# Kernel tuning notes

Measured on AMD Instinct MI355X. Metric: run time of the kernel, lower is better.

The kernel has to match this reference:

```python
import jax, jax.numpy as jnp
import numpy as np

INPUT_SIZE, HIDDEN_SIZE, MEMORY_SIZE, SEQ_LEN, THETA = 512, 1024, 256, 4096, 4096.0
BATCH = 8


def _expm(M):
    # scaling-and-squaring Taylor expm (float64), replaces scipy cont2discrete's expm
    nrm = np.linalg.norm(M, 1)
    s = max(0, int(np.ceil(np.log2(max(nrm, 1.0)))) + 4)
    A = M / (2.0 ** s)
    E = np.eye(M.shape[0])
    T = np.eye(M.shape[0])
    for k in range(1, 24):
        T = T @ A / k
        E = E + T
    for _ in range(s):
        E = E @ E
    return E


def _lmu_H():
    # continuous-time Legendre state-space matrices
    Q = np.arange(MEMORY_SIZE, dtype=np.float64).reshape(-1, 1)
    R = (2.0 * Q + 1.0) / THETA
    i, j = np.meshgrid(Q.ravel(), Q.ravel(), indexing="ij")
    A = R * np.where(i < j, -1.0, (-1.0) ** (i - j + 1))
    B = R * (-1.0) ** Q
    # zero-order-hold discretization with dt=1: expm([[A,B],[0,0]])
    aug = np.zeros((MEMORY_SIZE + 1, MEMORY_SIZE + 1))
    aug[:MEMORY_SIZE, :MEMORY_SIZE] = A
    aug[:MEMORY_SIZE, MEMORY_SIZE:] = B
    Md = _expm(aug)
    Ad = Md[:MEMORY_SIZE, :MEMORY_SIZE].astype(np.float32)
    Bd = Md[:MEMORY_SIZE, MEMORY_SIZE:].astype(np.float32)
    # impulse response: H[:, t] = Ad^t @ Bd  (matches torch impulse() in float32)
    H = np.empty((MEMORY_SIZE, SEQ_LEN), dtype=np.float32)
    h = Bd[:, 0]
    for t in range(SEQ_LEN):
        H[:, t] = h
        h = Ad @ h
    return H


def setup_inputs():
    key = jax.random.key(0)
    k1, k2, k3, k4, k5 = jax.random.split(key, 5)
    x = jax.random.normal(k1, (BATCH, SEQ_LEN, INPUT_SIZE), jnp.float32)
    W_u_w = jax.random.normal(k2, (1, INPUT_SIZE), jnp.float32) / np.float32(np.sqrt(INPUT_SIZE))
    W_u_b = jax.random.normal(k3, (1,), jnp.float32) * 0.01
    W_h_w = jax.random.normal(k4, (HIDDEN_SIZE, MEMORY_SIZE + INPUT_SIZE), jnp.float32) / np.float32(np.sqrt(MEMORY_SIZE + INPUT_SIZE))
    W_h_b = jax.random.normal(k5, (HIDDEN_SIZE,), jnp.float32) * 0.01
    H = jnp.asarray(_lmu_H())
    return {"x": x, "W_u_w": W_u_w, "W_u_b": W_u_b, "W_h_w": W_h_w, "W_h_b": W_h_b, "H": H}


def reference(x, W_u_w, W_u_b, W_h_w, W_h_b, H):
    B, S, D = x.shape
    # u_t = relu(W_u x_t)  -> [B, S, 1]
    u = jax.nn.relu(jnp.einsum("bsd,od->bso", x, W_u_w) + W_u_b)
    # FFT long convolution of u with impulse response H (linear conv via 2S padding)
    fft_u = jnp.fft.rfft(u.transpose(0, 2, 1), n=2 * S, axis=-1)  # [B, 1, S+1]
    fft_H = jnp.fft.rfft(H, n=2 * S, axis=-1)                     # [M, S+1]
    m = jnp.fft.irfft(fft_u * fft_H[None], n=2 * S, axis=-1)[:, :, :S]  # [B, M, S]
    m = m.transpose(0, 2, 1)                                      # [B, S, M]
    # h_t = relu(W_h [m_t; x_t])
    h = jax.nn.relu(jnp.einsum("bsk,hk->bsh", jnp.concatenate([m, x], axis=-1), W_h_w) + W_h_b)
    return h, h[:, -1, :]
```

## Files before the change

### kernel.cpp

```cpp
#include <hip/hip_runtime.h>

typedef _Float16 half8 __attribute__((ext_vector_type(8)));
typedef float f32x4 __attribute__((ext_vector_type(4)));

#define SEQ   4096
#define DIN   512
#define HID   1024
#define KMEM  256
#define NB    8
#define KC    768
#define VP    4352
#define OUT_H_ELEMS 33554432ull

__device__ __forceinline__ void load_lds16(const void* g, void* l) {
  __builtin_amdgcn_global_load_lds(
      (const __attribute__((address_space(1))) unsigned int*)g,
      (__attribute__((address_space(3))) unsigned int*)l, 16, 0, 0);
}

__global__ __launch_bounds__(256) void u_kernel(
    const float* __restrict__ x, const float* __restrict__ Wu,
    const float* __restrict__ Wub,
    const float* __restrict__ Hf, const float* __restrict__ Wf,
    _Float16* __restrict__ xh, _Float16* __restrict__ v2,
    _Float16* __restrict__ Hh, _Float16* __restrict__ Wh)
{
  int tid_g = blockIdx.x * 256 + threadIdx.x;
  if (tid_g < KMEM * SEQ) Hh[tid_g] = (_Float16)Hf[tid_g];
  if (tid_g < HID * KC)   Wh[tid_g] = (_Float16)Wf[tid_g];
  if (tid_g < NB * 8 * 256) {
    int b2 = tid_g >> 11, rem = tid_g & 2047, p = rem >> 8, z = rem & 255;
    int t = (z < p) ? z : 4096 + z;
    v2[((size_t)b2 * 8 + p) * VP + t] = (_Float16)0.f;
  }

  int w = threadIdx.x >> 6, lane = threadIdx.x & 63;
  int row = blockIdx.x * 4 + w;
  const float4* xr = (const float4*)(x + (size_t)row * DIN);
  const float4* wr = (const float4*)Wu;
  float4 a0 = xr[lane * 2], a1 = xr[lane * 2 + 1];
  float4 w0 = wr[lane * 2], w1 = wr[lane * 2 + 1];
  float dot = a0.x * w0.x + a0.y * w0.y + a0.z * w0.z + a0.w * w0.w
            + a1.x * w1.x + a1.y * w1.y + a1.z * w1.z + a1.w * w1.w;
  half8 hv;
  hv[0] = (_Float16)a0.x; hv[1] = (_Float16)a0.y;
  hv[2] = (_Float16)a0.z; hv[3] = (_Float16)a0.w;
  hv[4] = (_Float16)a1.x; hv[5] = (_Float16)a1.y;
  hv[6] = (_Float16)a1.z; hv[7] = (_Float16)a1.w;
  *((half8*)(xh + (size_t)row * DIN + lane * 8)) = hv;
  #pragma unroll
  for (int off = 32; off > 0; off >>= 1) dot += __shfl_xor(dot, off);
  float u = dot + Wub[0];
  u = u > 0.f ? u : 0.f;
  if (lane < 8) {
    int s = row & (SEQ - 1), b = row >> 12;
    v2[(size_t)b * 8 * VP + (size_t)lane * VP + (4095 - s + lane)] = (_Float16)u;
  }
}

__global__ __launch_bounds__(256, 3) void conv_kernel(
    const _Float16* __restrict__ Hh, const _Float16* __restrict__ v2,
    _Float16* __restrict__ mh)
{
  __shared__ _Float16 Bs[2][128 * 64];
  __shared__ _Float16 Aw[2][8 * 208];
  int g = blockIdx.x;
  int cb = g & 15;
  int b = cb >> 1, kt = cb & 1;
  int jj = g >> 4;
  int its = (jj < 16) ? jj : (47 - jj);
  int s0 = its * 128, k0 = kt * 128;
  int tid = threadIdx.x;
  int w = tid >> 6, lane = tid & 63;
  int wr = w >> 1, wc = w & 1;
  int lm = lane & 15, q = lane >> 4;
  const _Float16* v2b = v2 + (size_t)b * 8 * VP;
  int gb = 3968 - s0;

  int aoffs[4];
  #pragma unroll
  for (int mi = 0; mi < 4; mi++) {
    int X = wr * 64 + mi * 16 + lm;
    int p = (X + 1) & 7;
    aoffs[mi] = p * 208 + (127 - X + p) + q * 8;
  }
  int boffs[4];
  #pragma unroll
  for (int ni = 0; ni < 4; ni++) {
    int col = wc * 64 + ni * 16 + lm;
    boffs[ni] = col * 64 + ((q ^ (lm & 7)) << 3);
  }

  int ap = tid / 26, aidx = tid - ap * 26;

  f32x4 acc[4][4] = {};
  int iters = 2 * (its + 1);

  {
    if (tid < 208)
      load_lds16(v2b + (size_t)ap * VP + gb + aidx * 8, Aw[0] + tid * 8);
    #pragma unroll
    for (int p2 = 0; p2 < 4; p2++) {
      int c = p2 * 256 + tid;
      int col = c >> 3, sl = c & 7;
      load_lds16(Hh + (size_t)(k0 + col) * SEQ + ((sl ^ (col & 7)) << 3),
                 Bs[0] + (size_t)c * 8);
    }
  }

  for (int it = 0; it < iters; ++it) {
    int buf = it & 1;
    __syncthreads();
    if (it + 1 < iters) {
      int r0 = (it + 1) * 64;
      if (tid < 208)
        load_lds16(v2b + (size_t)ap * VP + gb + r0 + aidx * 8, Aw[buf ^ 1] + tid * 8);
      #pragma unroll
      for (int p2 = 0; p2 < 4; p2++) {
        int c = p2 * 256 + tid;
        int col = c >> 3, sl = c & 7;
        load_lds16(Hh + (size_t)(k0 + col) * SEQ + r0 + ((sl ^ (col & 7)) << 3),
                   Bs[buf ^ 1] + (size_t)c * 8);
      }
    }
    #pragma unroll
    for (int kq = 0; kq < 2; kq++) {
      half8 af[4], bf[4];
      #pragma unroll
      for (int mi = 0; mi < 4; mi++)
        af[mi] = *((const half8*)(Aw[buf] + aoffs[mi] + kq * 32));
      #pragma unroll
      for (int ni = 0; ni < 4; ni++)
        bf[ni] = *((const half8*)(Bs[buf] + (boffs[ni] ^ (kq << 5))));
      #pragma unroll
      for (int mi = 0; mi < 4; mi++)
        #pragma unroll
        for (int ni = 0; ni < 4; ni++)
          acc[mi][ni] = __builtin_amdgcn_mfma_f32_16x16x32_f16(af[mi], bf[ni], acc[mi][ni], 0, 0, 0);
    }
  }
  size_t rowbase = (size_t)b * SEQ;
  #pragma unroll
  for (int mi = 0; mi < 4; mi++) {
    #pragma unroll
    for (int ni = 0; ni < 4; ni++) {
      int kout = k0 + wc * 64 + ni * 16 + lm;
      #pragma unroll
      for (int r = 0; r < 4; r++) {
        int sout = s0 + wr * 64 + mi * 16 + q * 4 + r;
        mh[(rowbase + sout) * KMEM + kout] = (_Float16)acc[mi][ni][r];
      }
    }
  }
}

__global__ __launch_bounds__(256) void h_kernel(
    const _Float16* __restrict__ mh, const _Float16* __restrict__ xh,
    const _Float16* __restrict__ Wh, const float* __restrict__ Whb,
    float* __restrict__ out)
{
  __shared__ _Float16 As[2][128 * 32];
  __shared__ _Float16 Bs[2][128 * 32];
  int id = blockIdx.y * 8 + blockIdx.x;
  int xcd = id & 7;
  int j = id >> 3;
  int mt = (j >> 3) * 8 + xcd;
  int nt = j & 7;
  int tid = threadIdx.x, w = tid >> 6, lane = tid & 63;
  int wr = w >> 1, wc = w & 1, lm = lane & 15, q = lane >> 4;

  f32x4 acc[4][4] = {};
  {
    #pragma unroll
    for (int p2 = 0; p2 < 2; p2++) {
      int c = p2 * 256 + tid;
      int row = c >> 2, ch = c & 3;
      size_t rg = (size_t)mt * 128 + row;
      load_lds16(mh + rg * KMEM + ch * 8, As[0] + (size_t)c * 8);
      load_lds16(Wh + (size_t)(nt * 128 + row) * KC + ch * 8, Bs[0] + (size_t)c * 8);
    }
  }
  for (int it = 0; it < 24; ++it) {
    int buf = it & 1;
    __syncthreads();
    if (it + 1 < 24) {
      int kk = (it + 1) * 32;
      #pragma unroll
      for (int p2 = 0; p2 < 2; p2++) {
        int c = p2 * 256 + tid;
        int row = c >> 2, ch = c & 3;
        size_t rg = (size_t)mt * 128 + row;
        const _Float16* srcA = (kk < KMEM)
            ? (mh + rg * KMEM + kk + ch * 8)
            : (xh + rg * DIN + (kk - KMEM) + ch * 8);
        load_lds16(srcA, As[buf ^ 1] + (size_t)c * 8);
        load_lds16(Wh + (size_t)(nt * 128 + row) * KC + kk + ch * 8,
                   Bs[buf ^ 1] + (size_t)c * 8);
      }
    }
    half8 af[4], bf[4];
    #pragma unroll
    for (int mi = 0; mi < 4; mi++)
      af[mi] = *((const half8*)(As[buf] + (wr * 64 + mi * 16 + lm) * 32 + q * 8));
    #pragma unroll
    for (int ni = 0; ni < 4; ni++)
      bf[ni] = *((const half8*)(Bs[buf] + (wc * 64 + ni * 16 + lm) * 32 + q * 8));
    #pragma unroll
    for (int mi = 0; mi < 4; mi++)
      #pragma unroll
      for (int ni = 0; ni < 4; ni++)
        acc[mi][ni] = __builtin_amdgcn_mfma_f32_16x16x32_f16(af[mi], bf[ni], acc[mi][ni], 0, 0, 0);
  }
  #pragma unroll
  for (int ni = 0; ni < 4; ni++) {
    int colg = nt * 128 + wc * 64 + ni * 16 + lm;
    float bias = Whb[colg];
    #pragma unroll
    for (int mi = 0; mi < 4; mi++) {
      #pragma unroll
      for (int r = 0; r < 4; r++) {
        int rowg = mt * 128 + wr * 64 + mi * 16 + q * 4 + r;
        float v = acc[mi][ni][r] + bias;
        v = v > 0.f ? v : 0.f;
        out[(size_t)rowg * HID + colg] = v;
        if ((rowg & (SEQ - 1)) == SEQ - 1)
          out[OUT_H_ELEMS + (size_t)(rowg >> 12) * HID + colg] = v;
      }
    }
  }
}

extern "C" void kernel_launch(void* const* d_in, const int* in_sizes, int n_in,
                              void* d_out, int out_size, void* d_ws, size_t ws_size,
                              hipStream_t stream) {
  const float* x   = (const float*)d_in[0];
  const float* Wu  = (const float*)d_in[1];
  const float* Wub = (const float*)d_in[2];
  const float* Whw = (const float*)d_in[3];
  const float* Whb = (const float*)d_in[4];
  const float* Hf  = (const float*)d_in[5];
  float* out = (float*)d_out;

  char* ws = (char*)d_ws;
  _Float16* Hh = (_Float16*)(ws);
  _Float16* Wh = (_Float16*)(ws + 2097152);
  _Float16* v2 = (_Float16*)(ws + 3670016);
  _Float16* xh = (_Float16*)(ws + 4227072);
  _Float16* mh = (_Float16*)(ws + 37781504);

  u_kernel<<<dim3(8192), dim3(256), 0, stream>>>(x, Wu, Wub, Hf, Whw, xh, v2, Hh, Wh);
  conv_kernel<<<dim3(512), dim3(256), 0, stream>>>(Hh, v2, mh);
  h_kernel<<<dim3(8, 256), dim3(256), 0, stream>>>(mh, xh, Wh, Whb, out);
}
```

Measured before the change: 327.2 us.

## Enlarge h_kernel tile to 256x256 with 3-stage LDS pipeline

The output GEMM moves from 128x128 tiles with 256 threads to 256x256 tiles with 512 threads (8 waves, each computing 128x64). A triple-buffered LDS prefetch two stages ahead, explicit vmcnt waits and s_setprio around the MFMA block replace the old double buffer with __syncthreads. The aim is to raise arithmetic intensity per loaded byte and overlap global loads with MFMA work. The grid shrinks to 512 blocks, so occupancy drops and there is more register pressure from 32 accumulators per wave.

```diff
diff --git a/kernel.cpp b/kernel.cpp
--- a/kernel.cpp
+++ b/kernel.cpp
@@ -154,72 +154,92 @@
   }
 }
 
-__global__ __launch_bounds__(256) void h_kernel(
+__global__ __launch_bounds__(512, 2) void h_kernel(
     const _Float16* __restrict__ mh, const _Float16* __restrict__ xh,
     const _Float16* __restrict__ Wh, const float* __restrict__ Whb,
     float* __restrict__ out)
 {
-  __shared__ _Float16 As[2][128 * 32];
-  __shared__ _Float16 Bs[2][128 * 32];
-  int id = blockIdx.y * 8 + blockIdx.x;
-  int xcd = id & 7;
-  int j = id >> 3;
-  int mt = (j >> 3) * 8 + xcd;
-  int nt = j & 7;
-  int tid = threadIdx.x, w = tid >> 6, lane = tid & 63;
-  int wr = w >> 1, wc = w & 1, lm = lane & 15, q = lane >> 4;
-
-  f32x4 acc[4][4] = {};
-  {
-    #pragma unroll
-    for (int p2 = 0; p2 < 2; p2++) {
-      int c = p2 * 256 + tid;
-      int row = c >> 2, ch = c & 3;
-      size_t rg = (size_t)mt * 128 + row;
-      load_lds16(mh + rg * KMEM + ch * 8, As[0] + (size_t)c * 8);
-      load_lds16(Wh + (size_t)(nt * 128 + row) * KC + ch * 8, Bs[0] + (size_t)c * 8);
-    }
-  }
-  for (int it = 0; it < 24; ++it) {
-    int buf = it & 1;
-    __syncthreads();
-    if (it + 1 < 24) {
-      int kk = (it + 1) * 32;
-      #pragma unroll
-      for (int p2 = 0; p2 < 2; p2++) {
-        int c = p2 * 256 + tid;
-        int row = c >> 2, ch = c & 3;
-        size_t rg = (size_t)mt * 128 + row;
-        const _Float16* srcA = (kk < KMEM)
-            ? (mh + rg * KMEM + kk + ch * 8)
-            : (xh + rg * DIN + (kk - KMEM) + ch * 8);
-        load_lds16(srcA, As[buf ^ 1] + (size_t)c * 8);
-        load_lds16(Wh + (size_t)(nt * 128 + row) * KC + kk + ch * 8,
-                   Bs[buf ^ 1] + (size_t)c * 8);
-      }
-    }
-    half8 af[4], bf[4];
-    #pragma unroll
-    for (int mi = 0; mi < 4; mi++)
-      af[mi] = *((const half8*)(As[buf] + (wr * 64 + mi * 16 + lm) * 32 + q * 8));
-    #pragma unroll
-    for (int ni = 0; ni < 4; ni++)
-      bf[ni] = *((const half8*)(Bs[buf] + (wc * 64 + ni * 16 + lm) * 32 + q * 8));
-    #pragma unroll
-    for (int mi = 0; mi < 4; mi++)
-      #pragma unroll
-      for (int ni = 0; ni < 4; ni++)
+  __shared__ _Float16 A3[3][256 * 32];
+  __shared__ _Float16 B3[3][256 * 32];
+
+  int id = blockIdx.x;
+  int wgid = (id & 7) * 64 + (id >> 3);
+  int mt = wgid >> 2, nt = wgid & 3;
+
+  int tid = threadIdx.x;
+  int w = tid >> 6, lane = tid & 63;
+  int wr = w >> 2, wc = w & 3;
+  int lm = lane & 15, q = lane >> 4;
+
+  int offM[2], offX[2], offB[2], ldsc[2];
+  #pragma unroll
+  for (int r = 0; r < 2; ++r) {
+    int row = r * 128 + (tid >> 2);
+    int sl = tid & 3;
+    offM[r] = (mt * 256 + row) * KMEM + sl * 8;
+    offX[r] = (mt * 256 + row) * DIN  + sl * 8;
+    offB[r] = (nt * 256 + row) * KC   + sl * 8;
+    ldsc[r] = (r * 512 + tid) * 8;
+  }
+
+#define H_STAGE(t) do {                                                        \
+    const int kk_ = (t) * 32;                                                  \
+    _Float16* As_ = A3[(t) % 3];                                               \
+    _Float16* Bs_ = B3[(t) % 3];                                               \
+    _Pragma("unroll")                                                          \
+    for (int r_ = 0; r_ < 2; ++r_) {                                           \
+      const _Float16* sa_ = (kk_ < KMEM) ? (mh + offM[r_] + kk_)               \
+                                         : (xh + offX[r_] + (kk_ - KMEM));     \
+      load_lds16(sa_, As_ + ldsc[r_]);                                         \
+      load_lds16(Wh + offB[r_] + kk_, Bs_ + ldsc[r_]);                         \
+    }                                                                          \
+  } while (0)
+
+  f32x4 acc[8][4] = {};
+
+  H_STAGE(0); H_STAGE(1);
+  asm volatile("s_waitcnt vmcnt(4)" ::: "memory");
+  __builtin_amdgcn_s_barrier();
+  asm volatile("" ::: "memory");
+
+  #pragma unroll
+  for (int t = 0; t < 24; ++t) {
+    if (t + 2 < 24) H_STAGE(t + 2);
+    const _Float16* la = A3[t % 3];
+    const _Float16* lb = B3[t % 3];
+    half8 af[8], bf[4];
+    #pragma unroll
+    for (int mi = 0; mi < 8; ++mi)
+      af[mi] = *((const half8*)(la + (wr * 128 + mi * 16 + lm) * 32 + q * 8));
+    #pragma unroll
+    for (int ni = 0; ni < 4; ++ni)
+      bf[ni] = *((const half8*)(lb + (wc * 64 + ni * 16 + lm) * 32 + q * 8));
+    __builtin_amdgcn_s_setprio(1);
+    #pragma unroll
+    for (int mi = 0; mi < 8; ++mi)
+      #pragma unroll
+      for (int ni = 0; ni < 4; ++ni)
         acc[mi][ni] = __builtin_amdgcn_mfma_f32_16x16x32_f16(af[mi], bf[ni], acc[mi][ni], 0, 0, 0);
-  }
-  #pragma unroll
-  for (int ni = 0; ni < 4; ni++) {
-    int colg = nt * 128 + wc * 64 + ni * 16 + lm;
+    __builtin_amdgcn_s_setprio(0);
+    asm volatile("" ::: "memory");
+    if (t < 22)       asm volatile("s_waitcnt vmcnt(4)" ::: "memory");
+    else if (t == 22) asm volatile("s_waitcnt vmcnt(0)" ::: "memory");
+    if (t < 23) {
+      __builtin_amdgcn_s_barrier();
+      asm volatile("" ::: "memory");
+    }
+  }
+#undef H_STAGE
+
+  #pragma unroll
+  for (int ni = 0; ni < 4; ++ni) {
+    int colg = nt * 256 + wc * 64 + ni * 16 + lm;
     float bias = Whb[colg];
     #pragma unroll
-    for (int mi = 0; mi < 4; mi++) {
-      #pragma unroll
-      for (int r = 0; r < 4; r++) {
-        int rowg = mt * 128 + wr * 64 + mi * 16 + q * 4 + r;
+    for (int mi = 0; mi < 8; ++mi) {
+      #pragma unroll
+      for (int r = 0; r < 4; ++r) {
+        int rowg = mt * 256 + wr * 128 + mi * 16 + q * 4 + r;
         float v = acc[mi][ni][r] + bias;
         v = v > 0.f ? v : 0.f;
         out[(size_t)rowg * HID + colg] = v;
@@ -250,5 +270,5 @@
 
   u_kernel<<<dim3(8192), dim3(256), 0, stream>>>(x, Wu, Wub, Hf, Whw, xh, v2, Hh, Wh);
   conv_kernel<<<dim3(512), dim3(256), 0, stream>>>(Hh, v2, mh);
-  h_kernel<<<dim3(8, 256), dim3(256), 0, stream>>>(mh, xh, Wh, Whb, out);
-}
+  h_kernel<<<dim3(512), dim3(512), 0, stream>>>(mh, xh, Wh, Whb, out);
+}
```

Result: slower. 338.0 us (+3.3%).
